# Performance work log

Hardware: AMD Instinct MI355X
Metric: run time of the kernel (lower is better)

The kernel has to match this reference:

```python
import jax, jax.numpy as jnp
import numpy as np

N = 50000      # nodes
E = 160000     # edges
NFEAT = 1024
NHID = 512
NCLASS = 64


def _unif(k, shape, fan):
    s = 1.0 / np.sqrt(fan)
    return jax.random.uniform(k, shape, jnp.float32, -s, s)


def setup_inputs() -> dict:
    key = jax.random.key(0)
    ks = jax.random.split(key, 16)
    x = jax.random.normal(ks[0], (N, NFEAT), jnp.float32)
    adj_row = jax.random.randint(ks[1], (E,), 0, N, jnp.int32)
    adj_col = jax.random.randint(ks[2], (E,), 0, N, jnp.int32)
    adj_val = jax.random.uniform(ks[3], (E,), jnp.float32)
    # gc1: nfeat -> nhid (stdv = 1/sqrt(out_features))
    W1 = _unif(ks[4], (NFEAT, NHID), NHID)
    b1 = _unif(ks[5], (NHID,), NHID)
    # residual projection for gc1 (nn.Linear nfeat->nhid)
    p1W = _unif(ks[6], (NFEAT, NHID), NFEAT)
    p1b = _unif(ks[7], (NHID,), NFEAT)
    # gc3: nhid -> nhid (shared across 4 applications)
    W3 = _unif(ks[8], (NHID, NHID), NHID)
    b3 = _unif(ks[9], (NHID,), NHID)
    # gc2: nhid -> nclass
    W2 = _unif(ks[10], (NHID, NCLASS), NCLASS)
    b2 = _unif(ks[11], (NCLASS,), NCLASS)
    # residual projection for gc2 (nn.Linear nhid->nclass)
    p2W = _unif(ks[12], (NHID, NCLASS), NHID)
    p2b = _unif(ks[13], (NCLASS,), NHID)
    return {"x": x, "adj_row": adj_row, "adj_col": adj_col, "adj_val": adj_val,
            "W1": W1, "b1": b1, "p1W": p1W, "p1b": p1b,
            "W3": W3, "b3": b3, "W2": W2, "b2": b2, "p2W": p2W, "p2b": p2b}


def _spmm(row, col, val, support):
    # out[i] = sum_e val[e] * support[col[e]] for row[e] == i   (adj @ support)
    return jax.ops.segment_sum(val[:, None] * support[col], row, num_segments=N)


def reference(x, adj_row, adj_col, adj_val, W1, b1, p1W, p1b, W3, b3, W2, b2, p2W, p2b):
    def gc_proj(inp, W, b, pW, pb):
        # shapes differ -> projected residual
        out = _spmm(adj_row, adj_col, adj_val, inp @ W) + b
        return jax.nn.relu(out + inp @ pW + pb)

    def gc_res(inp, W, b):
        # same shape -> identity residual
        out = _spmm(adj_row, adj_col, adj_val, inp @ W) + b
        return jax.nn.relu(out + inp)

    h = jax.nn.relu(gc_proj(x, W1, b1, p1W, p1b))       # [N, NHID]
    for _ in range(4):                                   # gc3 shared weights x4
        h = jax.nn.relu(gc_res(h, W3, b3))
    h = gc_proj(h, W2, b2, p2W, p2b)                     # [N, NCLASS]
    return jax.nn.log_softmax(h, axis=1)
```

## Files before the change

kernel.cpp:

```cpp
#include <hip/hip_runtime.h>

typedef __attribute__((ext_vector_type(8))) short bf16x8;
typedef __attribute__((ext_vector_type(8))) unsigned short ushort8;
typedef __attribute__((ext_vector_type(4))) float f32x4;

#define NNODES 50000
#define NEDGES 160000
#define MP     50176
#define NB_SCAN 196

__device__ __forceinline__ float bf2f(unsigned short u) {
  return __uint_as_float(((unsigned int)u) << 16);
}
__device__ __forceinline__ unsigned short f2bf(float f) {
  unsigned int u = __float_as_uint(f);
  u += 0x7fffu + ((u >> 16) & 1u);
  return (unsigned short)(u >> 16);
}
__device__ __forceinline__ void gld16(const void* g, void* l) {
  __builtin_amdgcn_global_load_lds((__attribute__((address_space(1))) void*)g,
                                   (__attribute__((address_space(3))) void*)l, 16, 0, 0);
}

__global__ void k_hist(const int* __restrict__ row, int* __restrict__ cnt, int n) {
  int i = blockIdx.x * 256 + threadIdx.x;
  if (i < n) atomicAdd(&cnt[row[i]], 1);
}

__global__ void k_block_reduce(const int* __restrict__ cnt, int* __restrict__ bsum, int n) {
  __shared__ int sd[256];
  int i = blockIdx.x * 256 + threadIdx.x;
  sd[threadIdx.x] = (i < n) ? cnt[i] : 0;
  __syncthreads();
  for (int o = 128; o > 0; o >>= 1) {
    if (threadIdx.x < o) sd[threadIdx.x] += sd[threadIdx.x + o];
    __syncthreads();
  }
  if (threadIdx.x == 0) bsum[blockIdx.x] = sd[0];
}

__global__ void k_scan_bsum(const int* __restrict__ bsum, int* __restrict__ boff, int nb,
                            int* __restrict__ rowptr, int n, int E) {
  __shared__ int sd[256];
  int v = (threadIdx.x < nb) ? bsum[threadIdx.x] : 0;
  sd[threadIdx.x] = v;
  __syncthreads();
  for (int o = 1; o < 256; o <<= 1) {
    int t = (threadIdx.x >= o) ? sd[threadIdx.x - o] : 0;
    __syncthreads();
    sd[threadIdx.x] += t;
    __syncthreads();
  }
  if (threadIdx.x < nb) boff[threadIdx.x] = sd[threadIdx.x] - v;
  if (threadIdx.x == 0) rowptr[n] = E;
}

__global__ void k_block_scan(const int* __restrict__ cnt, const int* __restrict__ boff,
                             int* __restrict__ rowptr, int* __restrict__ cursor, int n) {
  __shared__ int sd[256];
  int i = blockIdx.x * 256 + threadIdx.x;
  int v = (i < n) ? cnt[i] : 0;
  sd[threadIdx.x] = v;
  __syncthreads();
  for (int o = 1; o < 256; o <<= 1) {
    int t = (threadIdx.x >= o) ? sd[threadIdx.x - o] : 0;
    __syncthreads();
    sd[threadIdx.x] += t;
    __syncthreads();
  }
  if (i < n) {
    int r = boff[blockIdx.x] + sd[threadIdx.x] - v;
    rowptr[i] = r;
    cursor[i] = r;
  }
}

__global__ void k_scatter(const int* __restrict__ row, const int* __restrict__ col,
                          const float* __restrict__ val, int* __restrict__ cursor,
                          int* __restrict__ scol, float* __restrict__ sval, int n) {
  int e = blockIdx.x * 256 + threadIdx.x;
  if (e < n) {
    int p = atomicAdd(&cursor[row[e]], 1);
    scol[p] = col[e];
    sval[p] = val[e];
  }
}

__global__ void k_cast_x(const float* __restrict__ x, unsigned short* __restrict__ xb, int nRealRows) {
  size_t idx = ((size_t)blockIdx.x * 256 + threadIdx.x) * 8;
  if (idx >= (size_t)MP * 1024) return;
  int row = (int)(idx >> 10);
  ushort8 o;
  if (row < nRealRows) {
    float4 a = *(const float4*)(x + idx);
    float4 b = *(const float4*)(x + idx + 4);
    o[0] = f2bf(a.x); o[1] = f2bf(a.y); o[2] = f2bf(a.z); o[3] = f2bf(a.w);
    o[4] = f2bf(b.x); o[5] = f2bf(b.y); o[6] = f2bf(b.z); o[7] = f2bf(b.w);
  } else {
    o = (ushort8){0,0,0,0,0,0,0,0};
  }
  *(ushort8*)(xb + idx) = o;
}

__global__ void k_packT(const float* __restrict__ src, int K, int srcW, int nc,
                        unsigned short* __restrict__ dst, int dstOff) {
  __shared__ float tile[32][33];
  int k0 = blockIdx.x * 32, n0 = blockIdx.y * 32;
  int tx = threadIdx.x, ty = threadIdx.y;
  for (int i = ty; i < 32; i += 8)
    tile[i][tx] = src[(size_t)(k0 + i) * srcW + (n0 + tx)];
  __syncthreads();
  for (int i = ty; i < 32; i += 8)
    dst[(size_t)(dstOff + n0 + i) * K + (k0 + tx)] = f2bf(tile[tx][i]);
}

__global__ void k_pack_bias(const float* __restrict__ b1, const float* __restrict__ p1b,
                            const float* __restrict__ b2, const float* __restrict__ p2b,
                            float* __restrict__ bias1, float* __restrict__ bias2) {
  int t = threadIdx.x;
  bias1[t] = b1[t] + p1b[t];
  if (t < 64) bias2[t] = b2[t] + p2b[t];
}

__global__ __launch_bounds__(512, 4) void k_gemm128x256(
    const unsigned short* __restrict__ A, const unsigned short* __restrict__ Bt,
    unsigned short* __restrict__ C, int M, int N, int K) {
  extern __shared__ char smem[];
  const int NT = N >> 8;
  const int nwg = gridDim.x;
  const int q = nwg >> 3, r = nwg & 7;
  const int xcd = blockIdx.x & 7, local = blockIdx.x >> 3;
  const int swz = (xcd < r ? xcd * (q + 1) : r * (q + 1) + (xcd - r) * q) + local;
  const int mt = swz / NT, nt = swz % NT;

  const int tid = threadIdx.x;
  const int w = tid >> 6, lane = tid & 63;
  const int wr = w >> 2, wc = w & 3;

  const int srow = tid >> 2;
  const int schunk = (tid & 3) ^ ((tid >> 3) & 3);
  const unsigned short* gA = A + (size_t)(mt * 128 + srow) * K + schunk * 8;
  const unsigned short* gB = Bt + (size_t)(nt * 256 + srow) * K + schunk * 8;
  const size_t rs128 = (size_t)128 * K;
  const int wb = w << 10;

  const int l15 = lane & 15;
  const int cpos = ((lane >> 4) ^ ((l15 >> 1) & 3)) << 4;
  const int aOff = (wr * 64 + l15) * 64 + cpos;
  const int bOff = 8192 + (wc * 64 + l15) * 64 + cpos;

  f32x4 acc[4][4] = {};
  const int T = K >> 5;

  auto STAGE = [&](int t) {
    char* db = smem + (t % 3) * 24576 + wb;
    const unsigned short* a = gA + t * 32;
    const unsigned short* b = gB + t * 32;
    gld16(a, db);
    gld16(b, db + 8192);
    gld16(b + rs128, db + 16384);
  };

  STAGE(0); STAGE(1);

  for (int t = 0; t < T; ++t) {
    if (t < T - 1) asm volatile("s_waitcnt vmcnt(3)" ::: "memory");
    else           asm volatile("s_waitcnt vmcnt(0)" ::: "memory");
    __builtin_amdgcn_s_barrier();
    __builtin_amdgcn_sched_barrier(0);
    if (t + 2 < T) STAGE(t + 2);
    const int bb = (t % 3) * 24576;
    bf16x8 af[4];
#pragma unroll
    for (int m = 0; m < 4; ++m) af[m] = *(const bf16x8*)(smem + bb + aOff + m * 1024);
    __builtin_amdgcn_s_setprio(1);
#pragma unroll
    for (int n = 0; n < 4; ++n) {
      bf16x8 bfr = *(const bf16x8*)(smem + bb + bOff + n * 1024);
#pragma unroll
      for (int m = 0; m < 4; ++m)
        acc[m][n] = __builtin_amdgcn_mfma_f32_16x16x32_bf16(af[m], bfr, acc[m][n], 0, 0, 0);
    }
    __builtin_amdgcn_s_setprio(0);
  }

  const int r0 = mt * 128 + wr * 64 + (lane >> 4) * 4;
  const int c0e = nt * 256 + wc * 64 + l15;
#pragma unroll
  for (int m = 0; m < 4; ++m)
#pragma unroll
    for (int n = 0; n < 4; ++n)
#pragma unroll
      for (int j = 0; j < 4; ++j)
        C[(size_t)(r0 + m * 16 + j) * N + (c0e + n * 16)] = f2bf(acc[m][n][j]);
}

__global__ __launch_bounds__(256) void k_gemm_bt(
    const unsigned short* __restrict__ A, const unsigned short* __restrict__ Bt,
    unsigned short* __restrict__ C, int M, int N, int K) {
  __shared__ __align__(16) unsigned short As[128 * 32];
  __shared__ __align__(16) unsigned short Bs[128 * 32];
  const int ntc = N >> 7;
  const int mt = blockIdx.x / ntc;
  const int nt = blockIdx.x % ntc;
  const int t = threadIdx.x;
  const int w = t >> 6, lane = t & 63;
  const int wr = w >> 1, wc = w & 1;
  f32x4 acc[4][4] = {};
  const unsigned short* ga = A + (size_t)(mt * 128 + (t >> 2)) * K + (t & 3) * 8;
  const unsigned short* gb = Bt + (size_t)(nt * 128 + (t >> 2)) * K + (t & 3) * 8;
  unsigned short* lA = &As[w * 512];
  unsigned short* lB = &Bs[w * 512];
  const size_t rowskip = (size_t)64 * K;
  for (int kt = 0; kt < K; kt += 32) {
    gld16(ga + kt, lA);
    gld16(ga + kt + rowskip, lA + 2048);
    gld16(gb + kt, lB);
    gld16(gb + kt + rowskip, lB + 2048);
    __syncthreads();
    bf16x8 af[4], bfr[4];
#pragma unroll
    for (int m = 0; m < 4; ++m)
      af[m] = *(const bf16x8*)&As[(wr * 64 + m * 16 + (lane & 15)) * 32 + (lane >> 4) * 8];
#pragma unroll
    for (int n = 0; n < 4; ++n)
      bfr[n] = *(const bf16x8*)&Bs[(wc * 64 + n * 16 + (lane & 15)) * 32 + (lane >> 4) * 8];
#pragma unroll
    for (int m = 0; m < 4; ++m)
#pragma unroll
      for (int n = 0; n < 4; ++n)
        acc[m][n] = __builtin_amdgcn_mfma_f32_16x16x32_bf16(af[m], bfr[n], acc[m][n], 0, 0, 0);
    __syncthreads();
  }
  const int r0 = mt * 128 + wr * 64 + (lane >> 4) * 4;
  const int c0 = nt * 128 + wc * 64 + (lane & 15);
#pragma unroll
  for (int m = 0; m < 4; ++m)
#pragma unroll
    for (int n = 0; n < 4; ++n)
#pragma unroll
      for (int r = 0; r < 4; ++r)
        C[(size_t)(r0 + m * 16 + r) * N + (c0 + n * 16)] = f2bf(acc[m][n][r]);
}

__global__ __launch_bounds__(256) void k_spmm_ep512(
    const int* __restrict__ rowptr, const int* __restrict__ scol, const float* __restrict__ sval,
    const unsigned short* __restrict__ s, int sStride,
    const unsigned short* __restrict__ res, int resStride,
    const float* __restrict__ bias,
    unsigned short* __restrict__ o, int oStride, int nReal, int nTot) {
  int gw = (blockIdx.x * 256 + threadIdx.x) >> 6;
  int lane = threadIdx.x & 63;
  if (gw >= nTot) return;
  unsigned short* op = o + (size_t)gw * oStride + lane * 8;
  if (gw >= nReal) {
    *(ushort8*)op = (ushort8){0,0,0,0,0,0,0,0};
    return;
  }
  float acc[8] = {0.f,0.f,0.f,0.f,0.f,0.f,0.f,0.f};
  int e0 = rowptr[gw], e1 = rowptr[gw + 1];
  for (int e = e0; e < e1; ++e) {
    int c = scol[e];
    float v = sval[e];
    ushort8 svv = *(const ushort8*)(s + (size_t)c * sStride + lane * 8);
#pragma unroll
    for (int k = 0; k < 8; ++k) acc[k] += v * bf2f(svv[k]);
  }
  ushort8 rv = *(const ushort8*)(res + (size_t)gw * resStride + lane * 8);
  ushort8 ov;
#pragma unroll
  for (int k = 0; k < 8; ++k) {
    float tt = acc[k] + bias[lane * 8 + k] + bf2f(rv[k]);
    ov[k] = f2bf(fmaxf(tt, 0.f));
  }
  *(ushort8*)op = ov;
}

__global__ __launch_bounds__(256) void k_spmm_lsm(
    const int* __restrict__ rowptr, const int* __restrict__ scol, const float* __restrict__ sval,
    const unsigned short* __restrict__ g2, const float* __restrict__ bias2,
    float* __restrict__ out, int n) {
  int gw = (blockIdx.x * 256 + threadIdx.x) >> 6;
  int lane = threadIdx.x & 63;
  if (gw >= n) return;
  int e0 = rowptr[gw], e1 = rowptr[gw + 1];
  float acc = 0.f;
  for (int e = e0; e < e1; ++e) {
    int c = scol[e];
    acc += sval[e] * bf2f(g2[(size_t)c * 128 + lane]);
  }
  float t = acc + bias2[lane] + bf2f(g2[(size_t)gw * 128 + 64 + lane]);
  float v = fmaxf(t, 0.f);
  float m = v;
#pragma unroll
  for (int o = 32; o > 0; o >>= 1) m = fmaxf(m, __shfl_xor(m, o));
  float ex = __expf(v - m);
  float ss = ex;
#pragma unroll
  for (int o = 32; o > 0; o >>= 1) ss += __shfl_xor(ss, o);
  out[(size_t)gw * 64 + lane] = v - m - __logf(ss);
}

extern "C" void kernel_launch(void* const* d_in, const int* in_sizes, int n_in,
                              void* d_out, int out_size, void* d_ws, size_t ws_size,
                              hipStream_t stream) {
  const float* x    = (const float*)d_in[0];
  const int*   arow = (const int*)d_in[1];
  const int*   acol = (const int*)d_in[2];
  const float* aval = (const float*)d_in[3];
  const float* W1   = (const float*)d_in[4];
  const float* b1   = (const float*)d_in[5];
  const float* p1W  = (const float*)d_in[6];
  const float* p1b  = (const float*)d_in[7];
  const float* W3   = (const float*)d_in[8];
  const float* b3   = (const float*)d_in[9];
  const float* W2   = (const float*)d_in[10];
  const float* b2   = (const float*)d_in[11];
  const float* p2W  = (const float*)d_in[12];
  const float* p2b  = (const float*)d_in[13];
  float* out = (float*)d_out;

  char* wsp = (char*)d_ws;
  size_t off = 0;
  auto take = [&](size_t bytes) -> char* {
    char* p = wsp + off;
    off = (off + bytes + 255) & ~(size_t)255;
    return p;
  };
  unsigned short* xb  = (unsigned short*)take((size_t)MP * 1024 * 2);
  unsigned short* g1  = (unsigned short*)take((size_t)MP * 1024 * 2);
  unsigned short* B1t = (unsigned short*)take((size_t)1024 * 1024 * 2);
  unsigned short* W3t = (unsigned short*)take((size_t)512 * 512 * 2);
  unsigned short* B2t = (unsigned short*)take((size_t)128 * 512 * 2);
  float* bias1 = (float*)take(512 * 4);
  float* bias2 = (float*)take(64 * 4);
  int*   cnt    = (int*)take((size_t)NNODES * 4);
  int*   rowptr = (int*)take((size_t)(NNODES + 1) * 4);
  int*   bsum   = (int*)take(256 * 4);
  int*   boff   = (int*)take(256 * 4);
  int*   scol   = (int*)take((size_t)NEDGES * 4);
  float* sval   = (float*)take((size_t)NEDGES * 4);
  unsigned short* h  = xb;
  unsigned short* s  = g1;
  unsigned short* g2 = g1;

  hipMemsetAsync(cnt, 0, (size_t)NNODES * 4, stream);
  k_hist<<<(NEDGES + 255) / 256, 256, 0, stream>>>(arow, cnt, NEDGES);
  k_block_reduce<<<NB_SCAN, 256, 0, stream>>>(cnt, bsum, NNODES);
  k_scan_bsum<<<1, 256, 0, stream>>>(bsum, boff, NB_SCAN, rowptr, NNODES, NEDGES);
  k_block_scan<<<NB_SCAN, 256, 0, stream>>>(cnt, boff, rowptr, cnt, NNODES);
  k_scatter<<<(NEDGES + 255) / 256, 256, 0, stream>>>(arow, acol, aval, cnt, scol, sval, NEDGES);

  k_cast_x<<<(int)(((size_t)MP * 1024 / 8 + 255) / 256), 256, 0, stream>>>(x, xb, NNODES);
  k_packT<<<dim3(1024 / 32, 512 / 32), dim3(32, 8), 0, stream>>>(W1, 1024, 512, 512, B1t, 0);
  k_packT<<<dim3(1024 / 32, 512 / 32), dim3(32, 8), 0, stream>>>(p1W, 1024, 512, 512, B1t, 512);
  k_packT<<<dim3(512 / 32, 512 / 32), dim3(32, 8), 0, stream>>>(W3, 512, 512, 512, W3t, 0);
  k_packT<<<dim3(512 / 32, 64 / 32), dim3(32, 8), 0, stream>>>(W2, 512, 64, 64, B2t, 0);
  k_packT<<<dim3(512 / 32, 64 / 32), dim3(32, 8), 0, stream>>>(p2W, 512, 64, 64, B2t, 64);
  k_pack_bias<<<1, 512, 0, stream>>>(b1, p1b, b2, p2b, bias1, bias2);

  k_gemm128x256<<<392 * 4, 512, 73728, stream>>>(xb, B1t, g1, MP, 1024, 1024);
  k_spmm_ep512<<<MP / 4, 256, 0, stream>>>(rowptr, scol, sval, g1, 1024, g1 + 512, 1024,
                                           bias1, h, 512, NNODES, MP);
  for (int i = 0; i < 4; ++i) {
    k_gemm128x256<<<392 * 2, 512, 73728, stream>>>(h, W3t, s, MP, 512, 512);
    k_spmm_ep512<<<MP / 4, 256, 0, stream>>>(rowptr, scol, sval, s, 512, h, 512,
                                             b3, h, 512, NNODES, MP);
  }
  k_gemm_bt<<<MP / 128, 256, 0, stream>>>(h, B2t, g2, MP, 128, 512);
  k_spmm_lsm<<<(NNODES + 3) / 4, 256, 0, stream>>>(rowptr, scol, sval, g2, bias2, out, NNODES);
}
```

Baseline: 614.6 us.

## Widen GEMM tile to 128x512, merge pack kernels, unroll SpMM edges by two

```diff
diff --git a/kernel.cpp b/kernel.cpp
--- a/kernel.cpp
+++ b/kernel.cpp
@@ -102,11 +102,33 @@
   *(ushort8*)(xb + idx) = o;
 }
 
-__global__ void k_packT(const float* __restrict__ src, int K, int srcW, int nc,
-                        unsigned short* __restrict__ dst, int dstOff) {
+__global__ void k_pack_all(const float* __restrict__ W1, const float* __restrict__ p1W,
+                           const float* __restrict__ W3, const float* __restrict__ W2,
+                           const float* __restrict__ p2W,
+                           const float* __restrict__ b1, const float* __restrict__ p1b,
+                           const float* __restrict__ b2, const float* __restrict__ p2b,
+                           unsigned short* __restrict__ B1t, unsigned short* __restrict__ W3t,
+                           unsigned short* __restrict__ B2t,
+                           float* __restrict__ bias1, float* __restrict__ bias2) {
+  int z = blockIdx.z;
+  int tx = threadIdx.x, ty = threadIdx.y;
+  if (z == 5) {
+    if (blockIdx.x || blockIdx.y) return;
+    int t = ty * 32 + tx;
+    bias1[t] = b1[t] + p1b[t];
+    bias1[t + 256] = b1[t + 256] + p1b[t + 256];
+    if (t < 64) bias2[t] = b2[t] + p2b[t];
+    return;
+  }
+  const float* src; unsigned short* dst; int K, srcW, nc, dstOff;
+  if (z == 0)      { src = W1;  dst = B1t; K = 1024; srcW = 512; nc = 512; dstOff = 0; }
+  else if (z == 1) { src = p1W; dst = B1t; K = 1024; srcW = 512; nc = 512; dstOff = 512; }
+  else if (z == 2) { src = W3;  dst = W3t; K = 512;  srcW = 512; nc = 512; dstOff = 0; }
+  else if (z == 3) { src = W2;  dst = B2t; K = 512;  srcW = 64;  nc = 64;  dstOff = 0; }
+  else             { src = p2W; dst = B2t; K = 512;  srcW = 64;  nc = 64;  dstOff = 64; }
+  int k0 = blockIdx.x * 32, n0 = blockIdx.y * 32;
+  if (k0 >= K || n0 >= nc) return;
   __shared__ float tile[32][33];
-  int k0 = blockIdx.x * 32, n0 = blockIdx.y * 32;
-  int tx = threadIdx.x, ty = threadIdx.y;
   for (int i = ty; i < 32; i += 8)
     tile[i][tx] = src[(size_t)(k0 + i) * srcW + (n0 + tx)];
   __syncthreads();
@@ -114,19 +136,11 @@
     dst[(size_t)(dstOff + n0 + i) * K + (k0 + tx)] = f2bf(tile[tx][i]);
 }
 
-__global__ void k_pack_bias(const float* __restrict__ b1, const float* __restrict__ p1b,
-                            const float* __restrict__ b2, const float* __restrict__ p2b,
-                            float* __restrict__ bias1, float* __restrict__ bias2) {
-  int t = threadIdx.x;
-  bias1[t] = b1[t] + p1b[t];
-  if (t < 64) bias2[t] = b2[t] + p2b[t];
-}
-
-__global__ __launch_bounds__(512, 4) void k_gemm128x256(
+__global__ __launch_bounds__(512, 4) void k_gemm_w64x128(
     const unsigned short* __restrict__ A, const unsigned short* __restrict__ Bt,
     unsigned short* __restrict__ C, int M, int N, int K) {
   extern __shared__ char smem[];
-  const int NT = N >> 8;
+  const int NT = N >> 9;
   const int nwg = gridDim.x;
   const int q = nwg >> 3, r = nwg & 7;
   const int xcd = blockIdx.x & 7, local = blockIdx.x >> 3;
@@ -140,42 +154,41 @@
   const int srow = tid >> 2;
   const int schunk = (tid & 3) ^ ((tid >> 3) & 3);
   const unsigned short* gA = A + (size_t)(mt * 128 + srow) * K + schunk * 8;
-  const unsigned short* gB = Bt + (size_t)(nt * 256 + srow) * K + schunk * 8;
+  const unsigned short* gB = Bt + (size_t)(nt * 512 + srow) * K + schunk * 8;
   const size_t rs128 = (size_t)128 * K;
   const int wb = w << 10;
 
   const int l15 = lane & 15;
   const int cpos = ((lane >> 4) ^ ((l15 >> 1) & 3)) << 4;
   const int aOff = (wr * 64 + l15) * 64 + cpos;
-  const int bOff = 8192 + (wc * 64 + l15) * 64 + cpos;
-
-  f32x4 acc[4][4] = {};
+  const int bOff = 8192 + (wc * 128 + l15) * 64 + cpos;
+
+  f32x4 acc[4][8] = {};
   const int T = K >> 5;
 
   auto STAGE = [&](int t) {
-    char* db = smem + (t % 3) * 24576 + wb;
+    char* db = smem + (t & 1) * 40960 + wb;
     const unsigned short* a = gA + t * 32;
     const unsigned short* b = gB + t * 32;
     gld16(a, db);
     gld16(b, db + 8192);
     gld16(b + rs128, db + 16384);
+    gld16(b + 2 * rs128, db + 24576);
+    gld16(b + 3 * rs128, db + 32768);
   };
 
-  STAGE(0); STAGE(1);
-
+  STAGE(0);
   for (int t = 0; t < T; ++t) {
-    if (t < T - 1) asm volatile("s_waitcnt vmcnt(3)" ::: "memory");
-    else           asm volatile("s_waitcnt vmcnt(0)" ::: "memory");
+    asm volatile("s_waitcnt vmcnt(0)" ::: "memory");
     __builtin_amdgcn_s_barrier();
-    __builtin_amdgcn_sched_barrier(0);
-    if (t + 2 < T) STAGE(t + 2);
-    const int bb = (t % 3) * 24576;
+    if (t + 1 < T) STAGE(t + 1);
+    const int bb = (t & 1) * 40960;
     bf16x8 af[4];
 #pragma unroll
     for (int m = 0; m < 4; ++m) af[m] = *(const bf16x8*)(smem + bb + aOff + m * 1024);
     __builtin_amdgcn_s_setprio(1);
 #pragma unroll
-    for (int n = 0; n < 4; ++n) {
+    for (int n = 0; n < 8; ++n) {
       bf16x8 bfr = *(const bf16x8*)(smem + bb + bOff + n * 1024);
 #pragma unroll
       for (int m = 0; m < 4; ++m)
@@ -185,11 +198,11 @@
   }
 
   const int r0 = mt * 128 + wr * 64 + (lane >> 4) * 4;
-  const int c0e = nt * 256 + wc * 64 + l15;
+  const int c0e = nt * 512 + wc * 128 + l15;
 #pragma unroll
   for (int m = 0; m < 4; ++m)
 #pragma unroll
-    for (int n = 0; n < 4; ++n)
+    for (int n = 0; n < 8; ++n)
 #pragma unroll
       for (int j = 0; j < 4; ++j)
         C[(size_t)(r0 + m * 16 + j) * N + (c0e + n * 16)] = f2bf(acc[m][n][j]);
@@ -259,12 +272,21 @@
   }
   float acc[8] = {0.f,0.f,0.f,0.f,0.f,0.f,0.f,0.f};
   int e0 = rowptr[gw], e1 = rowptr[gw + 1];
-  for (int e = e0; e < e1; ++e) {
+  int e = e0;
+  for (; e + 2 <= e1; e += 2) {
+    int c0 = scol[e], c1 = scol[e + 1];
+    float v0 = sval[e], v1 = sval[e + 1];
+    ushort8 s0 = *(const ushort8*)(s + (size_t)c0 * sStride + lane * 8);
+    ushort8 s1 = *(const ushort8*)(s + (size_t)c1 * sStride + lane * 8);
+#pragma unroll
+    for (int k = 0; k < 8; ++k) acc[k] += v0 * bf2f(s0[k]) + v1 * bf2f(s1[k]);
+  }
+  if (e < e1) {
     int c = scol[e];
     float v = sval[e];
-    ushort8 svv = *(const ushort8*)(s + (size_t)c * sStride + lane * 8);
-#pragma unroll
-    for (int k = 0; k < 8; ++k) acc[k] += v * bf2f(svv[k]);
+    ushort8 sv = *(const ushort8*)(s + (size_t)c * sStride + lane * 8);
+#pragma unroll
+    for (int k = 0; k < 8; ++k) acc[k] += v * bf2f(sv[k]);
   }
   ushort8 rv = *(const ushort8*)(res + (size_t)gw * resStride + lane * 8);
   ushort8 ov;
@@ -352,18 +374,15 @@
   k_scatter<<<(NEDGES + 255) / 256, 256, 0, stream>>>(arow, acol, aval, cnt, scol, sval, NEDGES);
 
   k_cast_x<<<(int)(((size_t)MP * 1024 / 8 + 255) / 256), 256, 0, stream>>>(x, xb, NNODES);
-  k_packT<<<dim3(1024 / 32, 512 / 32), dim3(32, 8), 0, stream>>>(W1, 1024, 512, 512, B1t, 0);
-  k_packT<<<dim3(1024 / 32, 512 / 32), dim3(32, 8), 0, stream>>>(p1W, 1024, 512, 512, B1t, 512);
-  k_packT<<<dim3(512 / 32, 512 / 32), dim3(32, 8), 0, stream>>>(W3, 512, 512, 512, W3t, 0);
-  k_packT<<<dim3(512 / 32, 64 / 32), dim3(32, 8), 0, stream>>>(W2, 512, 64, 64, B2t, 0);
-  k_packT<<<dim3(512 / 32, 64 / 32), dim3(32, 8), 0, stream>>>(p2W, 512, 64, 64, B2t, 64);
-  k_pack_bias<<<1, 512, 0, stream>>>(b1, p1b, b2, p2b, bias1, bias2);
-
-  k_gemm128x256<<<392 * 4, 512, 73728, stream>>>(xb, B1t, g1, MP, 1024, 1024);
+  k_pack_all<<<dim3(32, 16, 6), dim3(32, 8), 0, stream>>>(W1, p1W, W3, W2, p2W,
+                                                          b1, p1b, b2, p2b,
+                                                          B1t, W3t, B2t, bias1, bias2);
+
+  k_gemm_w64x128<<<392 * 2, 512, 81920, stream>>>(xb, B1t, g1, MP, 1024, 1024);
   k_spmm_ep512<<<MP / 4, 256, 0, stream>>>(rowptr, scol, sval, g1, 1024, g1 + 512, 1024,
                                            bias1, h, 512, NNODES, MP);
   for (int i = 0; i < 4; ++i) {
-    k_gemm128x256<<<392 * 2, 512, 73728, stream>>>(h, W3t, s, MP, 512, 512);
+    k_gemm_w64x128<<<392, 512, 81920, stream>>>(h, W3t, s, MP, 512, 512);
     k_spmm_ep512<<<MP / 4, 256, 0, stream>>>(rowptr, scol, sval, s, 512, h, 512,
                                              b3, h, 512, NNODES, MP);
   }
```

Measured after the change: 1.896 ms. +208.5%, slower.
